# Performance work log

Hardware: AMD Instinct MI355X
Metric: run time of the kernel (lower is better)

## Reference

```python
import jax, jax.numpy as jnp
import numpy as np
import math

D_MODEL = 1024
NUM_HEADS = 16
D_K = D_MODEL // NUM_HEADS
SEQ = 4096
BATCH = 1
NUM_BUCKETS = 32
MAX_DISTANCE = 4096


def _relative_position_bucket(relative_position):
    # T5-style unidirectional bucketing (only k < q gets nonzero bucket)
    n = jnp.maximum(-relative_position, 0)
    max_exact = NUM_BUCKETS // 2
    is_small = n < max_exact
    nf = jnp.maximum(n, 1).astype(jnp.float32)  # avoid log(0); masked by is_small
    val_if_large = max_exact + (
        jnp.log(nf / max_exact) / math.log(MAX_DISTANCE / max_exact) * (NUM_BUCKETS - max_exact)
    ).astype(jnp.int32)
    val_if_large = jnp.minimum(val_if_large, NUM_BUCKETS - 1)
    return jnp.where(is_small, n, val_if_large)


def setup_inputs() -> dict:
    key = jax.random.key(0)
    ks = jax.random.split(key, 12)
    s = 1.0 / math.sqrt(D_MODEL)
    inp = {
        "query": jax.random.normal(ks[0], (BATCH, SEQ, D_MODEL), jnp.float32),
        "key": jax.random.normal(ks[1], (BATCH, SEQ, D_MODEL), jnp.float32),
        "value": jax.random.normal(ks[2], (BATCH, SEQ, D_MODEL), jnp.float32),
        # causal mask: True where attention is forbidden (j > i)
        "mask": jnp.triu(jnp.ones((SEQ, SEQ), bool), k=1)[None, None],
        "Wq": jax.random.normal(ks[3], (D_MODEL, D_MODEL), jnp.float32) * s,
        "bq": jnp.zeros((D_MODEL,), jnp.float32),
        "Wk": jax.random.normal(ks[4], (D_MODEL, D_MODEL), jnp.float32) * s,
        "bk": jnp.zeros((D_MODEL,), jnp.float32),
        "Wv": jax.random.normal(ks[5], (D_MODEL, D_MODEL), jnp.float32) * s,
        "bv": jnp.zeros((D_MODEL,), jnp.float32),
        "Wo": jax.random.normal(ks[6], (D_MODEL, D_MODEL), jnp.float32) * s,
        "bo": jnp.zeros((D_MODEL,), jnp.float32),
        "rpe_table": jax.random.normal(ks[7], (NUM_BUCKETS, NUM_HEADS), jnp.float32),
    }
    return inp


def reference(query, key, value, mask, Wq, bq, Wk, bk, Wv, bv, Wo, bo, rpe_table):
    B, S, _ = query.shape
    scale = jnp.sqrt(jnp.asarray(D_K, jnp.float32))

    def heads(x, W, b):  # [B,S,D] -> [B,H,S,dk]
        return (x @ W + b).reshape(B, S, NUM_HEADS, D_K).transpose(0, 2, 1, 3)

    Q = heads(query, Wq, bq)
    K = heads(key, Wk, bk)
    V = heads(value, Wv, bv)

    energy = jnp.einsum("bhqd,bhkd->bhqk", Q, K) / scale

    pos = jnp.arange(S)
    rel = pos[None, :] - pos[:, None]              # [S,S] = k_pos - q_pos
    bucket = _relative_position_bucket(rel)        # [S,S] int
    bias = rpe_table[bucket]                       # [S,S,H]
    energy = energy + bias.transpose(2, 0, 1)[None]  # [1,H,S,S]

    neg = jnp.finfo(energy.dtype).min
    energy = jnp.where(mask, neg, energy)

    attn = jax.nn.softmax(energy, axis=-1)         # dropout p=0 -> identity
    x = jnp.einsum("bhqk,bhkd->bhqd", attn, V)
    x = x.transpose(0, 2, 1, 3).reshape(B, S, D_MODEL)
    return x @ Wo + bo
```

## Files before the change

kernel.cpp:

```cpp
#include <hip/hip_runtime.h>
#include <hip/hip_bf16.h>
#include <stdint.h>

using bf16   = __hip_bfloat16;
using bf16x8 = __attribute__((ext_vector_type(8))) short;
using bf16x4 = __attribute__((ext_vector_type(4))) short;
using f32x4  = __attribute__((ext_vector_type(4))) float;

__device__ __forceinline__ bf16x8 load8(const float* p) {
  f32x4 a = *(const f32x4*)p;
  f32x4 b = *(const f32x4*)(p + 4);
  bf16x8 r;
  bf16* rp = (bf16*)&r;
#pragma unroll
  for (int j = 0; j < 4; ++j) rp[j]     = __float2bfloat16(a[j]);
#pragma unroll
  for (int j = 0; j < 4; ++j) rp[4 + j] = __float2bfloat16(b[j]);
  return r;
}
__device__ __forceinline__ bf16x8 load8(const bf16* p) { return *(const bf16x8*)p; }

__global__ __launch_bounds__(256)
void transpose_w(const float* __restrict__ w0, const float* __restrict__ w1,
                 const float* __restrict__ w2, const float* __restrict__ w3,
                 bf16* __restrict__ o0, bf16* __restrict__ o1,
                 bf16* __restrict__ o2, bf16* __restrict__ o3)
{
  __shared__ float tile[32][33];
  int z = blockIdx.z;
  const float* in = (z == 0) ? w0 : (z == 1) ? w1 : (z == 2) ? w2 : w3;
  bf16* out       = (z == 0) ? o0 : (z == 1) ? o1 : (z == 2) ? o2 : o3;
  int bx = blockIdx.x * 32, by = blockIdx.y * 32;
  int tx = threadIdx.x & 31, ty = threadIdx.x >> 5;
#pragma unroll
  for (int i = 0; i < 4; ++i)
    tile[ty + i * 8][tx] = in[(size_t)(by + ty + i * 8) * 1024 + bx + tx];
  __syncthreads();
#pragma unroll
  for (int i = 0; i < 4; ++i)
    out[(size_t)(bx + ty + i * 8) * 1024 + by + tx] = __float2bfloat16(tile[tx][ty + i * 8]);
}

__global__ __launch_bounds__(256)
void build_bias(const float* __restrict__ rpe, float* __restrict__ bias_tab)
{
  int idx = blockIdx.x * 256 + threadIdx.x;
  int d = idx >> 4, h = idx & 15;
  int b;
  if (d < 16) {
    b = d;
  } else {
    const int T[15] = {23, 32, 46, 64, 91, 128, 182, 256, 363, 512,
                       725, 1024, 1449, 2048, 2897};
    int m = 0;
#pragma unroll
    for (int i = 0; i < 15; ++i) m += (d >= T[i]);
    b = 16 + m;
  }
  bias_tab[h * 4096 + d] = rpe[b * 16 + h];
}

template <typename AT, typename OT, bool VT>
__device__ __forceinline__ void gemm_body(const AT* __restrict__ A,
                                          const bf16* __restrict__ Wt,
                                          const float* __restrict__ bias,
                                          OT* __restrict__ C)
{
  __shared__ bf16 As[128 * 64];
  __shared__ bf16 Bs[128 * 64];
  const int tid = threadIdx.x;
  const int lane = tid & 63, wid = tid >> 6;
  const int l15 = lane & 15, lg = lane >> 4;
  const int wr = wid >> 1, wc = wid & 1;
  const int m0 = blockIdx.x * 128, n0 = blockIdx.y * 128;

  f32x4 acc[4][4];
#pragma unroll
  for (int i = 0; i < 4; ++i)
#pragma unroll
    for (int j = 0; j < 4; ++j) acc[i][j] = (f32x4){0.f, 0.f, 0.f, 0.f};

#pragma unroll 1
  for (int kt = 0; kt < 16; ++kt) {
    const int k0 = kt * 64;
    __syncthreads();
    bf16x8 ra[4], rb[4];
#pragma unroll
    for (int it = 0; it < 4; ++it) {
      const int ci = tid + it * 256;
      const int row = ci >> 3, s = ci & 7;
      ra[it] = load8(A  + (size_t)(m0 + row) * 1024 + k0 + s * 8);
      rb[it] = load8(Wt + (size_t)(n0 + row) * 1024 + k0 + s * 8);
    }
#pragma unroll
    for (int it = 0; it < 4; ++it) {
      const int ci = tid + it * 256;
      const int row = ci >> 3, s = ci & 7;
      const int off = row * 128 + ((s ^ (row & 7)) << 4);
      *(bf16x8*)((char*)As + off) = ra[it];
      *(bf16x8*)((char*)Bs + off) = rb[it];
    }
    __syncthreads();

    bf16x8 af[2][4], bfr[2][4];
#pragma unroll
    for (int ks = 0; ks < 2; ++ks) {
      const int s8 = ks * 4 + lg;
#pragma unroll
      for (int f = 0; f < 4; ++f) {
        const int ra_ = wr * 64 + f * 16 + l15;
        af[ks][f]  = *(const bf16x8*)((const char*)As + ra_ * 128 + ((s8 ^ (ra_ & 7)) << 4));
        const int rb_ = wc * 64 + f * 16 + l15;
        bfr[ks][f] = *(const bf16x8*)((const char*)Bs + rb_ * 128 + ((s8 ^ (rb_ & 7)) << 4));
      }
    }
#pragma unroll
    for (int ks = 0; ks < 2; ++ks)
#pragma unroll
      for (int mf = 0; mf < 4; ++mf)
#pragma unroll
        for (int nf = 0; nf < 4; ++nf)
          acc[mf][nf] = __builtin_amdgcn_mfma_f32_16x16x32_bf16(
              af[ks][mf], bfr[ks][nf], acc[mf][nf], 0, 0, 0);
  }

#pragma unroll
  for (int nf = 0; nf < 4; ++nf) {
    const int col = n0 + wc * 64 + nf * 16 + l15;
    const float bv = bias[col];
#pragma unroll
    for (int mf = 0; mf < 4; ++mf) {
      const int rowb = m0 + wr * 64 + mf * 16 + lg * 4;
#pragma unroll
      for (int r = 0; r < 4; ++r) {
        const float val = acc[mf][nf][r] + bv;
        if (VT) {
          ((bf16*)C)[((size_t)(col >> 6) << 18) + ((size_t)(col & 63) << 12) + rowb + r] =
              __float2bfloat16(val);
        } else if (sizeof(OT) == 4) {
          ((float*)C)[(size_t)(rowb + r) * 1024 + col] = val;
        } else {
          ((bf16*)C)[(size_t)(rowb + r) * 1024 + col] = __float2bfloat16(val);
        }
      }
    }
  }
}

__global__ __launch_bounds__(256)
void gemm_qk(const float* __restrict__ xq, const float* __restrict__ xk,
             const bf16* __restrict__ wqt, const bf16* __restrict__ wkt,
             const float* __restrict__ bq, const float* __restrict__ bk,
             bf16* __restrict__ Q, bf16* __restrict__ K)
{
  int z = blockIdx.z;
  gemm_body<float, bf16, false>(z == 0 ? xq : xk, z == 0 ? wqt : wkt,
                                z == 0 ? bq : bk, z == 0 ? Q : K);
}

__global__ __launch_bounds__(256)
void gemm_v(const float* __restrict__ xv, const bf16* __restrict__ wvt,
            const float* __restrict__ bv, bf16* __restrict__ VtG)
{
  gemm_body<float, bf16, true>(xv, wvt, bv, VtG);
}

__global__ __launch_bounds__(256)
void gemm_out(const bf16* __restrict__ A, const bf16* __restrict__ Wt,
              const float* __restrict__ bias, float* __restrict__ C)
{
  gemm_body<bf16, float, false>(A, Wt, bias, C);
}

__global__ __launch_bounds__(256)
void attn_kernel(const bf16* __restrict__ Qb, const bf16* __restrict__ Kb,
                 const bf16* __restrict__ VtG, const float* __restrict__ bias_tab,
                 bf16* __restrict__ Ob)
{
  __shared__ bf16 Ks[64 * 64];
  __shared__ bf16 Vs[64 * 64];
  __shared__ bf16 Pl[4][16 * 76];

  const int tid = threadIdx.x;
  const int lane = tid & 63, wid = tid >> 6;
  const int l15 = lane & 15, lg = lane >> 4;
  const int bid = blockIdx.x;
  const int h  = bid & 15;
  const int qt = 63 - (bid >> 4);
  const int nt = qt + 1;
  const int qw = qt * 64 + wid * 16;
  const int q_abs = qw + l15;

  const bf16* Kh = Kb + h * 64;
  const bf16* Vh = VtG + ((size_t)h << 18);
  const float* bh = bias_tab + h * 4096;
  bf16* pw = &Pl[wid][0];

  const int kr0 = tid >> 3, ks0_ = tid & 7;
  const int kr1 = (tid + 256) >> 3, ks1_ = tid & 7;

  bf16x8 qf[2];
  {
    const bf16* qp = Qb + (size_t)q_abs * 1024 + h * 64 + lg * 8;
    qf[0] = *(const bf16x8*)qp;
    qf[1] = *(const bf16x8*)(qp + 32);
  }

  f32x4 o_acc[4];
#pragma unroll
  for (int nf = 0; nf < 4; ++nf) o_acc[nf] = (f32x4){0.f, 0.f, 0.f, 0.f};
  float m_run = -1e30f, l_run = 0.f;

  bf16x8 rk0 = *(const bf16x8*)(Kh + (size_t)kr0 * 1024 + ks0_ * 8);
  bf16x8 rk1 = *(const bf16x8*)(Kh + (size_t)kr1 * 1024 + ks1_ * 8);
  bf16x8 rv0 = *(const bf16x8*)(Vh + (size_t)kr0 * 4096 + ks0_ * 8);
  bf16x8 rv1 = *(const bf16x8*)(Vh + (size_t)kr1 * 4096 + ks1_ * 8);

#pragma unroll 1
  for (int t = 0; t < nt; ++t) {
    const int k0 = t * 64;
    __syncthreads();
    {
      const int o0 = kr0 * 128 + ((ks0_ ^ (kr0 & 7)) << 4);
      const int o1 = kr1 * 128 + ((ks1_ ^ (kr1 & 7)) << 4);
      *(bf16x8*)((char*)Ks + o0) = rk0;
      *(bf16x8*)((char*)Ks + o1) = rk1;
      *(bf16x8*)((char*)Vs + o0) = rv0;
      *(bf16x8*)((char*)Vs + o1) = rv1;
    }
    __syncthreads();
    if (t + 1 < nt) {
      const int k1 = k0 + 64;
      rk0 = *(const bf16x8*)(Kh + (size_t)(k1 + kr0) * 1024 + ks0_ * 8);
      rk1 = *(const bf16x8*)(Kh + (size_t)(k1 + kr1) * 1024 + ks1_ * 8);
      rv0 = *(const bf16x8*)(Vh + (size_t)kr0 * 4096 + k1 + ks0_ * 8);
      rv1 = *(const bf16x8*)(Vh + (size_t)kr1 * 4096 + k1 + ks1_ * 8);
    }

    f32x4 st[4];
#pragma unroll
    for (int kf = 0; kf < 4; ++kf) st[kf] = (f32x4){0.f, 0.f, 0.f, 0.f};
#pragma unroll
    for (int kf = 0; kf < 4; ++kf) {
      const int row = kf * 16 + l15;
#pragma unroll
      for (int ks = 0; ks < 2; ++ks) {
        const int s8 = ks * 4 + lg;
        bf16x8 kfr = *(const bf16x8*)((const char*)Ks + row * 128 + ((s8 ^ (row & 7)) << 4));
        st[kf] = __builtin_amdgcn_mfma_f32_16x16x32_bf16(kfr, qf[ks], st[kf], 0, 0, 0);
      }
    }

    float bvr[4][4];
#pragma unroll
    for (int kf = 0; kf < 4; ++kf)
#pragma unroll
      for (int r = 0; r < 4; ++r) {
        const int d = q_abs - (k0 + kf * 16 + lg * 4 + r);
        bvr[kf][r] = (d >= 0) ? bh[d] : -1e30f;
      }

    float mt = -1e30f;
#pragma unroll
    for (int kf = 0; kf < 4; ++kf)
#pragma unroll
      for (int r = 0; r < 4; ++r) {
        const float sv = st[kf][r] * 0.125f + bvr[kf][r];
        st[kf][r] = sv;
        mt = fmaxf(mt, sv);
      }
    mt = fmaxf(mt, __shfl_xor(mt, 16, 64));
    mt = fmaxf(mt, __shfl_xor(mt, 32, 64));

    const float newm = fmaxf(m_run, mt);
    const float sc = (m_run > -1e29f) ? __expf(m_run - newm) : 0.f;
    m_run = newm;

    float rs = 0.f;
    bf16x4 pk[4];
#pragma unroll
    for (int kf = 0; kf < 4; ++kf)
#pragma unroll
      for (int r = 0; r < 4; ++r) {
        const float p = (st[kf][r] > -1e29f) ? __expf(st[kf][r] - newm) : 0.f;
        ((bf16*)&pk[kf])[r] = __float2bfloat16(p);
        rs += p;
      }
    rs += __shfl_xor(rs, 16, 64);
    rs += __shfl_xor(rs, 32, 64);
    l_run = l_run * sc + rs;

#pragma unroll
    for (int kf = 0; kf < 4; ++kf)
      *(bf16x4*)&pw[l15 * 76 + kf * 16 + lg * 4] = pk[kf];

    float scr[4];
#pragma unroll
    for (int r = 0; r < 4; ++r) scr[r] = __shfl(sc, lg * 4 + r, 64);
#pragma unroll
    for (int nf = 0; nf < 4; ++nf)
#pragma unroll
      for (int r = 0; r < 4; ++r) o_acc[nf][r] *= scr[r];

    bf16x8 pf[2];
#pragma unroll
    for (int ks2 = 0; ks2 < 2; ++ks2)
      pf[ks2] = *(const bf16x8*)&pw[l15 * 76 + ks2 * 32 + lg * 8];
#pragma unroll
    for (int ks2 = 0; ks2 < 2; ++ks2)
#pragma unroll
      for (int nf = 0; nf < 4; ++nf) {
        const int row = nf * 16 + l15;
        const int s8 = ks2 * 4 + lg;
        bf16x8 vfr = *(const bf16x8*)((const char*)Vs + row * 128 + ((s8 ^ (row & 7)) << 4));
        o_acc[nf] = __builtin_amdgcn_mfma_f32_16x16x32_bf16(pf[ks2], vfr, o_acc[nf], 0, 0, 0);
      }
  }

  const float linv = 1.f / l_run;
  float lr[4];
#pragma unroll
  for (int r = 0; r < 4; ++r) lr[r] = __shfl(linv, lg * 4 + r, 64);
#pragma unroll
  for (int nf = 0; nf < 4; ++nf)
#pragma unroll
    for (int r = 0; r < 4; ++r) {
      const int row = qw + lg * 4 + r;
      Ob[(size_t)row * 1024 + h * 64 + nf * 16 + l15] =
          __float2bfloat16(o_acc[nf][r] * lr[r]);
    }
}

extern "C" void kernel_launch(void* const* d_in, const int* in_sizes, int n_in,
                              void* d_out, int out_size, void* d_ws, size_t ws_size,
                              hipStream_t stream) {
  (void)in_sizes; (void)n_in; (void)out_size; (void)ws_size;
  const float* q   = (const float*)d_in[0];
  const float* k   = (const float*)d_in[1];
  const float* v   = (const float*)d_in[2];
  const float* Wq  = (const float*)d_in[4];
  const float* bq  = (const float*)d_in[5];
  const float* Wk  = (const float*)d_in[6];
  const float* bk  = (const float*)d_in[7];
  const float* Wv  = (const float*)d_in[8];
  const float* bv  = (const float*)d_in[9];
  const float* Wo  = (const float*)d_in[10];
  const float* bo  = (const float*)d_in[11];
  const float* rpe = (const float*)d_in[12];
  float* out = (float*)d_out;

  char* ws = (char*)d_ws;
  bf16* WqT = (bf16*)(ws + (size_t)0);
  bf16* WkT = (bf16*)(ws + ((size_t)2 << 20));
  bf16* WvT = (bf16*)(ws + ((size_t)4 << 20));
  bf16* WoT = (bf16*)(ws + ((size_t)6 << 20));
  bf16* Qb  = (bf16*)(ws + ((size_t)8 << 20));
  bf16* Kb  = (bf16*)(ws + ((size_t)16 << 20));
  bf16* VtG = (bf16*)(ws + ((size_t)24 << 20));
  bf16* Ob  = (bf16*)(ws + ((size_t)32 << 20));
  float* bias_tab = (float*)(ws + ((size_t)40 << 20));

  transpose_w<<<dim3(32, 32, 4), 256, 0, stream>>>(Wq, Wk, Wv, Wo, WqT, WkT, WvT, WoT);
  build_bias<<<dim3(256), 256, 0, stream>>>(rpe, bias_tab);
  gemm_qk<<<dim3(32, 8, 2), 256, 0, stream>>>(q, k, WqT, WkT, bq, bk, Qb, Kb);
  gemm_v<<<dim3(32, 8), 256, 0, stream>>>(v, WvT, bv, VtG);
  attn_kernel<<<dim3(1024), 256, 0, stream>>>(Qb, Kb, VtG, bias_tab, Ob);
  gemm_out<<<dim3(32, 8), 256, 0, stream>>>(Ob, WoT, bo, out);
}
```

Baseline: 374.5 us.

## Pre-convert inputs to bf16, use direct global-to-LDS loads, exp2 softmax with lazy rescale

Adds a separate kernel that converts the fp32 activations to bf16. The Q, K and V projections are merged into one launch, and their GEMM tiles are loaded straight into LDS with global_load_lds instead of going through registers. The bias table is padded and pre-scaled by log2(e) so attention can read it with vector loads and use exp2f. The running-max rescale is skipped unless the max grows by more than a threshold, and s_setprio is set around the MFMA sections. The extra conversion pass costs memory traffic, and the lazy rescale depends on a numerical margin to stay accurate.

```diff
diff --git a/kernel.cpp b/kernel.cpp
--- a/kernel.cpp
+++ b/kernel.cpp
@@ -6,6 +6,13 @@
 using bf16x8 = __attribute__((ext_vector_type(8))) short;
 using bf16x4 = __attribute__((ext_vector_type(4))) short;
 using f32x4  = __attribute__((ext_vector_type(4))) float;
+using f32x4a = __attribute__((ext_vector_type(4), aligned(4))) float;
+
+__device__ __forceinline__ void g2l16(const void* g, void* l) {
+  __builtin_amdgcn_global_load_lds(
+      (const __attribute__((address_space(1))) void*)g,
+      (__attribute__((address_space(3))) void*)l, 16, 0, 0);
+}
 
 __device__ __forceinline__ bf16x8 load8(const float* p) {
   f32x4 a = *(const f32x4*)p;
@@ -18,7 +25,18 @@
   for (int j = 0; j < 4; ++j) rp[4 + j] = __float2bfloat16(b[j]);
   return r;
 }
-__device__ __forceinline__ bf16x8 load8(const bf16* p) { return *(const bf16x8*)p; }
+
+__global__ __launch_bounds__(256)
+void cvt_bf16(const float* __restrict__ a, const float* __restrict__ b,
+              const float* __restrict__ c, bf16* __restrict__ oa,
+              bf16* __restrict__ ob, bf16* __restrict__ oc)
+{
+  const int z = blockIdx.z;
+  const float* src = (z == 0) ? a : (z == 1) ? b : c;
+  bf16* dst        = (z == 0) ? oa : (z == 1) ? ob : oc;
+  const int i = (blockIdx.x * 256 + threadIdx.x) * 8;
+  *(bf16x8*)(dst + i) = load8(src + i);
+}
 
 __global__ __launch_bounds__(256)
 void transpose_w(const float* __restrict__ w0, const float* __restrict__ w1,
@@ -42,32 +60,37 @@
 }
 
 __global__ __launch_bounds__(256)
-void build_bias(const float* __restrict__ rpe, float* __restrict__ bias_tab)
+void build_bias(const float* __restrict__ rpe, float* __restrict__ bt)
 {
   int idx = blockIdx.x * 256 + threadIdx.x;
-  int d = idx >> 4, h = idx & 15;
-  int b;
-  if (d < 16) {
-    b = d;
-  } else {
-    const int T[15] = {23, 32, 46, 64, 91, 128, 182, 256, 363, 512,
-                       725, 1024, 1449, 2048, 2897};
-    int m = 0;
-#pragma unroll
-    for (int i = 0; i < 15; ++i) m += (d >= T[i]);
-    b = 16 + m;
-  }
-  bias_tab[h * 4096 + d] = rpe[b * 16 + h];
-}
-
-template <typename AT, typename OT, bool VT>
-__device__ __forceinline__ void gemm_body(const AT* __restrict__ A,
+  if (idx >= 16 * 4104) return;
+  int h = idx / 4104, j = idx - h * 4104;
+  int d = j - 3;
+  float v = 0.f;
+  if (d >= 0 && d < 4096) {
+    int b;
+    if (d < 16) {
+      b = d;
+    } else {
+      const int T[15] = {23, 32, 46, 64, 91, 128, 182, 256, 363, 512,
+                         725, 1024, 1449, 2048, 2897};
+      int m = 0;
+#pragma unroll
+      for (int i = 0; i < 15; ++i) m += (d >= T[i]);
+      b = 16 + m;
+    }
+    v = rpe[b * 16 + h] * 1.4426950408889634f;
+  }
+  bt[idx] = v;
+}
+
+template <typename OT>
+__device__ __forceinline__ void gemm_body(const bf16* __restrict__ A,
                                           const bf16* __restrict__ Wt,
                                           const float* __restrict__ bias,
-                                          OT* __restrict__ C)
-{
-  __shared__ bf16 As[128 * 64];
-  __shared__ bf16 Bs[128 * 64];
+                                          OT* __restrict__ C, bool vt,
+                                          bf16* As, bf16* Bs)
+{
   const int tid = threadIdx.x;
   const int lane = tid & 63, wid = tid >> 6;
   const int l15 = lane & 15, lg = lane >> 4;
@@ -84,21 +107,13 @@
   for (int kt = 0; kt < 16; ++kt) {
     const int k0 = kt * 64;
     __syncthreads();
-    bf16x8 ra[4], rb[4];
 #pragma unroll
     for (int it = 0; it < 4; ++it) {
-      const int ci = tid + it * 256;
-      const int row = ci >> 3, s = ci & 7;
-      ra[it] = load8(A  + (size_t)(m0 + row) * 1024 + k0 + s * 8);
-      rb[it] = load8(Wt + (size_t)(n0 + row) * 1024 + k0 + s * 8);
-    }
-#pragma unroll
-    for (int it = 0; it < 4; ++it) {
-      const int ci = tid + it * 256;
-      const int row = ci >> 3, s = ci & 7;
-      const int off = row * 128 + ((s ^ (row & 7)) << 4);
-      *(bf16x8*)((char*)As + off) = ra[it];
-      *(bf16x8*)((char*)Bs + off) = rb[it];
+      const int o = tid * 16 + it * 4096;
+      const int row = o >> 7;
+      const int sl = ((o >> 4) & 7) ^ (row & 7);
+      g2l16(A  + (size_t)(m0 + row) * 1024 + k0 + sl * 8, (char*)As + wid * 1024 + it * 4096);
+      g2l16(Wt + (size_t)(n0 + row) * 1024 + k0 + sl * 8, (char*)Bs + wid * 1024 + it * 4096);
     }
     __syncthreads();
 
@@ -134,13 +149,14 @@
 #pragma unroll
       for (int r = 0; r < 4; ++r) {
         const float val = acc[mf][nf][r] + bv;
-        if (VT) {
-          ((bf16*)C)[((size_t)(col >> 6) << 18) + ((size_t)(col & 63) << 12) + rowb + r] =
-              __float2bfloat16(val);
-        } else if (sizeof(OT) == 4) {
+        if constexpr (sizeof(OT) == 2) {
+          if (vt)
+            ((bf16*)C)[((size_t)(col >> 6) << 18) + ((size_t)(col & 63) << 12) + rowb + r] =
+                __float2bfloat16(val);
+          else
+            ((bf16*)C)[(size_t)(rowb + r) * 1024 + col] = __float2bfloat16(val);
+        } else {
           ((float*)C)[(size_t)(rowb + r) * 1024 + col] = val;
-        } else {
-          ((bf16*)C)[(size_t)(rowb + r) * 1024 + col] = __float2bfloat16(val);
         }
       }
     }
@@ -148,28 +164,28 @@
 }
 
 __global__ __launch_bounds__(256)
-void gemm_qk(const float* __restrict__ xq, const float* __restrict__ xk,
-             const bf16* __restrict__ wqt, const bf16* __restrict__ wkt,
-             const float* __restrict__ bq, const float* __restrict__ bk,
-             bf16* __restrict__ Q, bf16* __restrict__ K)
-{
-  int z = blockIdx.z;
-  gemm_body<float, bf16, false>(z == 0 ? xq : xk, z == 0 ? wqt : wkt,
-                                z == 0 ? bq : bk, z == 0 ? Q : K);
-}
-
-__global__ __launch_bounds__(256)
-void gemm_v(const float* __restrict__ xv, const bf16* __restrict__ wvt,
-            const float* __restrict__ bv, bf16* __restrict__ VtG)
-{
-  gemm_body<float, bf16, true>(xv, wvt, bv, VtG);
-}
-
-__global__ __launch_bounds__(256)
-void gemm_out(const bf16* __restrict__ A, const bf16* __restrict__ Wt,
-              const float* __restrict__ bias, float* __restrict__ C)
-{
-  gemm_body<bf16, float, false>(A, Wt, bias, C);
+void gemm_qkv(const bf16* __restrict__ xq, const bf16* __restrict__ xk,
+              const bf16* __restrict__ xv,
+              const bf16* __restrict__ wqt, const bf16* __restrict__ wkt,
+              const bf16* __restrict__ wvt,
+              const float* __restrict__ bq, const float* __restrict__ bk,
+              const float* __restrict__ bv,
+              bf16* __restrict__ Q, bf16* __restrict__ K, bf16* __restrict__ VtG)
+{
+  __shared__ bf16 As[128 * 64], Bs[128 * 64];
+  const int z = blockIdx.z;
+  gemm_body<bf16>(z == 0 ? xq : z == 1 ? xk : xv,
+                  z == 0 ? wqt : z == 1 ? wkt : wvt,
+                  z == 0 ? bq : z == 1 ? bk : bv,
+                  z == 0 ? Q : z == 1 ? K : VtG, z == 2, As, Bs);
+}
+
+__global__ __launch_bounds__(256)
+void gemm_out_k(const bf16* __restrict__ A, const bf16* __restrict__ Wt,
+                const float* __restrict__ bias, float* __restrict__ C)
+{
+  __shared__ bf16 As[128 * 64], Bs[128 * 64];
+  gemm_body<float>(A, Wt, bias, C, false, As, Bs);
 }
 
 __global__ __launch_bounds__(256)
@@ -190,10 +206,11 @@
   const int nt = qt + 1;
   const int qw = qt * 64 + wid * 16;
   const int q_abs = qw + l15;
+  const float C1 = 0.125f * 1.4426950408889634f;
 
   const bf16* Kh = Kb + h * 64;
   const bf16* Vh = VtG + ((size_t)h << 18);
-  const float* bh = bias_tab + h * 4096;
+  const float* bh = bias_tab + h * 4104 + 3;
   bf16* pw = &Pl[wid][0];
 
   const int kr0 = tid >> 3, ks0_ = tid & 7;
@@ -240,6 +257,7 @@
     f32x4 st[4];
 #pragma unroll
     for (int kf = 0; kf < 4; ++kf) st[kf] = (f32x4){0.f, 0.f, 0.f, 0.f};
+    __builtin_amdgcn_s_setprio(1);
 #pragma unroll
     for (int kf = 0; kf < 4; ++kf) {
       const int row = kf * 16 + l15;
@@ -250,31 +268,38 @@
         st[kf] = __builtin_amdgcn_mfma_f32_16x16x32_bf16(kfr, qf[ks], st[kf], 0, 0, 0);
       }
     }
-
-    float bvr[4][4];
-#pragma unroll
-    for (int kf = 0; kf < 4; ++kf)
+    __builtin_amdgcn_s_setprio(0);
+
+    float mt = -1e30f;
+#pragma unroll
+    for (int kf = 0; kf < 4; ++kf) {
+      const int dtop = q_abs - (k0 + kf * 16 + lg * 4);
+      f32x4a b4 = (f32x4a){0.f, 0.f, 0.f, 0.f};
+      if (dtop >= 0) b4 = *(const f32x4a*)(bh + dtop - 3);
 #pragma unroll
       for (int r = 0; r < 4; ++r) {
-        const int d = q_abs - (k0 + kf * 16 + lg * 4 + r);
-        bvr[kf][r] = (d >= 0) ? bh[d] : -1e30f;
-      }
-
-    float mt = -1e30f;
-#pragma unroll
-    for (int kf = 0; kf < 4; ++kf)
-#pragma unroll
-      for (int r = 0; r < 4; ++r) {
-        const float sv = st[kf][r] * 0.125f + bvr[kf][r];
+        const float bb = (dtop - r >= 0) ? b4[3 - r] : -1e30f;
+        const float sv = st[kf][r] * C1 + bb;
         st[kf][r] = sv;
         mt = fmaxf(mt, sv);
       }
+    }
     mt = fmaxf(mt, __shfl_xor(mt, 16, 64));
     mt = fmaxf(mt, __shfl_xor(mt, 32, 64));
 
-    const float newm = fmaxf(m_run, mt);
-    const float sc = (m_run > -1e29f) ? __expf(m_run - newm) : 0.f;
-    m_run = newm;
+    if (__any(mt > m_run + 11.0f)) {
+      const float newm = fmaxf(m_run, mt);
+      const float sc = (m_run > -1e29f) ? exp2f(m_run - newm) : 0.f;
+      m_run = newm;
+      float scr[4];
+#pragma unroll
+      for (int r = 0; r < 4; ++r) scr[r] = __shfl(sc, lg * 4 + r, 64);
+#pragma unroll
+      for (int nf = 0; nf < 4; ++nf)
+#pragma unroll
+        for (int r = 0; r < 4; ++r) o_acc[nf][r] *= scr[r];
+      l_run *= sc;
+    }
 
     float rs = 0.f;
     bf16x4 pk[4];
@@ -282,30 +307,23 @@
     for (int kf = 0; kf < 4; ++kf)
 #pragma unroll
       for (int r = 0; r < 4; ++r) {
-        const float p = (st[kf][r] > -1e29f) ? __expf(st[kf][r] - newm) : 0.f;
+        const float p = (st[kf][r] > -1e29f) ? exp2f(st[kf][r] - m_run) : 0.f;
         ((bf16*)&pk[kf])[r] = __float2bfloat16(p);
         rs += p;
       }
     rs += __shfl_xor(rs, 16, 64);
     rs += __shfl_xor(rs, 32, 64);
-    l_run = l_run * sc + rs;
+    l_run += rs;
 
 #pragma unroll
     for (int kf = 0; kf < 4; ++kf)
       *(bf16x4*)&pw[l15 * 76 + kf * 16 + lg * 4] = pk[kf];
 
-    float scr[4];
-#pragma unroll
-    for (int r = 0; r < 4; ++r) scr[r] = __shfl(sc, lg * 4 + r, 64);
-#pragma unroll
-    for (int nf = 0; nf < 4; ++nf)
-#pragma unroll
-      for (int r = 0; r < 4; ++r) o_acc[nf][r] *= scr[r];
-
     bf16x8 pf[2];
 #pragma unroll
     for (int ks2 = 0; ks2 < 2; ++ks2)
       pf[ks2] = *(const bf16x8*)&pw[l15 * 76 + ks2 * 32 + lg * 8];
+    __builtin_amdgcn_s_setprio(1);
 #pragma unroll
     for (int ks2 = 0; ks2 < 2; ++ks2)
 #pragma unroll
@@ -315,6 +333,7 @@
         bf16x8 vfr = *(const bf16x8*)((const char*)Vs + row * 128 + ((s8 ^ (row & 7)) << 4));
         o_acc[nf] = __builtin_amdgcn_mfma_f32_16x16x32_bf16(pf[ks2], vfr, o_acc[nf], 0, 0, 0);
       }
+    __builtin_amdgcn_s_setprio(0);
   }
 
   const float linv = 1.f / l_run;
@@ -350,20 +369,24 @@
   float* out = (float*)d_out;
 
   char* ws = (char*)d_ws;
-  bf16* WqT = (bf16*)(ws + (size_t)0);
-  bf16* WkT = (bf16*)(ws + ((size_t)2 << 20));
-  bf16* WvT = (bf16*)(ws + ((size_t)4 << 20));
-  bf16* WoT = (bf16*)(ws + ((size_t)6 << 20));
-  bf16* Qb  = (bf16*)(ws + ((size_t)8 << 20));
-  bf16* Kb  = (bf16*)(ws + ((size_t)16 << 20));
-  bf16* VtG = (bf16*)(ws + ((size_t)24 << 20));
-  bf16* Ob  = (bf16*)(ws + ((size_t)32 << 20));
-  float* bias_tab = (float*)(ws + ((size_t)40 << 20));
+  bf16* WqT   = (bf16*)(ws + (size_t)0);
+  bf16* WkT   = (bf16*)(ws + ((size_t)2  << 20));
+  bf16* WvT   = (bf16*)(ws + ((size_t)4  << 20));
+  bf16* WoT   = (bf16*)(ws + ((size_t)6  << 20));
+  bf16* xq_bf = (bf16*)(ws + ((size_t)8  << 20));
+  bf16* xk_bf = (bf16*)(ws + ((size_t)16 << 20));
+  bf16* xv_bf = (bf16*)(ws + ((size_t)24 << 20));
+  bf16* Qb    = (bf16*)(ws + ((size_t)32 << 20));
+  bf16* Kb    = (bf16*)(ws + ((size_t)40 << 20));
+  bf16* VtG   = (bf16*)(ws + ((size_t)48 << 20));
+  float* bias_tab = (float*)(ws + ((size_t)56 << 20));
+  bf16* Ob    = xq_bf;
 
   transpose_w<<<dim3(32, 32, 4), 256, 0, stream>>>(Wq, Wk, Wv, Wo, WqT, WkT, WvT, WoT);
-  build_bias<<<dim3(256), 256, 0, stream>>>(rpe, bias_tab);
-  gemm_qk<<<dim3(32, 8, 2), 256, 0, stream>>>(q, k, WqT, WkT, bq, bk, Qb, Kb);
-  gemm_v<<<dim3(32, 8), 256, 0, stream>>>(v, WvT, bv, VtG);
+  build_bias<<<dim3(257), 256, 0, stream>>>(rpe, bias_tab);
+  cvt_bf16<<<dim3(2048, 1, 3), 256, 0, stream>>>(q, k, v, xq_bf, xk_bf, xv_bf);
+  gemm_qkv<<<dim3(32, 8, 3), 256, 0, stream>>>(xq_bf, xk_bf, xv_bf, WqT, WkT, WvT,
+                                               bq, bk, bv, Qb, Kb, VtG);
   attn_kernel<<<dim3(1024), 256, 0, stream>>>(Qb, Kb, VtG, bias_tab, Ob);
-  gemm_out<<<dim3(32, 8), 256, 0, stream>>>(Ob, WoT, bo, out);
-}
+  gemm_out_k<<<dim3(32, 8), 256, 0, stream>>>(Ob, WoT, bo, out);
+}
```

Result: faster. 355.5 us (-5.1%).
